# Performance work log

Measured on AMD Instinct MI355X. Metric: run time of the kernel, lower is better.

## Reference

```python
import jax, jax.numpy as jnp
import numpy as np

DIM = 128
HALF = DIM // 2
K = 8
B_TAIL = 1.0
MIN_W = 1e-3
MIN_H = 1e-3
MIN_D = 1e-3


def _fcnn(x, w1, b1, w2, b2, w3, b3):
    h = jax.nn.silu(x @ w1 + b1)
    h = jax.nn.silu(h @ w2 + b2)
    return h @ w3 + b3


def _rqs_forward(x, uw, uh, ud):
    # x: (B, D); uw/uh: (B, D, K); ud: (B, D, K-1)
    inside = (x >= -B_TAIL) & (x <= B_TAIL)
    const = np.log(np.exp(1.0 - MIN_D) - 1.0).astype(np.float32)
    ud = jnp.pad(ud, ((0, 0), (0, 0), (1, 1)), constant_values=const)

    widths = jax.nn.softmax(uw, axis=-1)
    widths = MIN_W + (1.0 - MIN_W * K) * widths
    cumw = jnp.pad(jnp.cumsum(widths, axis=-1), ((0, 0), (0, 0), (1, 0)))
    cumw = 2.0 * B_TAIL * cumw - B_TAIL
    cumw = cumw.at[..., 0].set(-B_TAIL).at[..., -1].set(B_TAIL)
    widths = cumw[..., 1:] - cumw[..., :-1]

    derivs = MIN_D + jax.nn.softplus(ud)

    heights = jax.nn.softmax(uh, axis=-1)
    heights = MIN_H + (1.0 - MIN_H * K) * heights
    cumh = jnp.pad(jnp.cumsum(heights, axis=-1), ((0, 0), (0, 0), (1, 0)))
    cumh = 2.0 * B_TAIL * cumh - B_TAIL
    cumh = cumh.at[..., 0].set(-B_TAIL).at[..., -1].set(B_TAIL)
    heights = cumh[..., 1:] - cumh[..., :-1]

    # searchsorted on cumwidths (forward direction)
    locs = cumw.at[..., -1].add(1e-6)
    idx = jnp.sum(x[..., None] >= locs, axis=-1) - 1
    idx = jnp.clip(idx, 0, K - 1)[..., None]  # (B, D, 1)

    g = lambda a: jnp.take_along_axis(a, idx, axis=-1)[..., 0]
    in_cumw = g(cumw)
    in_w = g(widths)
    in_cumh = g(cumh)
    in_h = g(heights)
    in_delta = g(heights / widths)
    d0 = g(derivs)
    d1 = g(derivs[..., 1:])

    theta = (x - in_cumw) / in_w
    t1mt = theta * (1.0 - theta)
    numer = in_h * (in_delta * theta * theta + d0 * t1mt)
    denom = in_delta + (d0 + d1 - 2.0 * in_delta) * t1mt
    out = in_cumh + numer / denom
    dnum = in_delta * in_delta * (d1 * theta * theta + 2.0 * in_delta * t1mt + d0 * (1.0 - theta) ** 2)
    lad = jnp.log(dnum) - 2.0 * jnp.log(denom)

    out = jnp.where(inside, out, x)
    lad = jnp.where(inside, lad, 0.0)
    return out, lad


def _forward(x, f1, f2):
    lower, upper = x[:, :HALF], x[:, HALF:]
    out = _fcnn(lower, *f1).reshape(-1, DIM - HALF, 3 * K - 1)
    W, H, D = out[..., :K], out[..., K:2 * K], out[..., 2 * K:]
    upper, ld1 = _rqs_forward(upper, W, H, D)
    out = _fcnn(upper, *f2).reshape(-1, HALF, 3 * K - 1)
    W, H, D = out[..., :K], out[..., K:2 * K], out[..., 2 * K:]
    lower, ld2 = _rqs_forward(lower, W, H, D)
    log_det = jnp.sum(ld1, axis=1) + jnp.sum(ld2, axis=1)
    return jnp.concatenate([lower, upper], axis=1), log_det


def setup_inputs() -> dict:
    key = jax.random.key(0)
    ks = jax.random.split(key, 13)
    batch = 32768
    x = jax.random.uniform(ks[0], (batch, DIM), jnp.float32, -1.2, 1.2)
    hd = 512
    out_dim = (3 * K - 1) * HALF  # 1472

    def lin(k, fan_in, fan_out):
        bound = 1.0 / np.sqrt(fan_in)
        kw, kb = jax.random.split(k)
        w = jax.random.uniform(kw, (fan_in, fan_out), jnp.float32, -bound, bound)
        b = jax.random.uniform(kb, (fan_out,), jnp.float32, -bound, bound)
        return w, b

    f1_w1, f1_b1 = lin(ks[1], HALF, hd)
    f1_w2, f1_b2 = lin(ks[2], hd, hd)
    f1_w3, f1_b3 = lin(ks[3], hd, out_dim)
    f2_w1, f2_b1 = lin(ks[4], HALF, hd)
    f2_w2, f2_b2 = lin(ks[5], hd, hd)
    f2_w3, f2_b3 = lin(ks[6], hd, out_dim)
    return dict(x=x,
                f1_w1=f1_w1, f1_b1=f1_b1, f1_w2=f1_w2, f1_b2=f1_b2, f1_w3=f1_w3, f1_b3=f1_b3,
                f2_w1=f2_w1, f2_b1=f2_b1, f2_w2=f2_w2, f2_b2=f2_b2, f2_w3=f2_w3, f2_b3=f2_b3)


def reference(x, f1_w1, f1_b1, f1_w2, f1_b2, f1_w3, f1_b3,
              f2_w1, f2_b1, f2_w2, f2_b2, f2_w3, f2_b3):
    f1 = (f1_w1, f1_b1, f1_w2, f1_b2, f1_w3, f1_b3)
    f2 = (f2_w1, f2_b1, f2_w2, f2_b2, f2_w3, f2_b3)
    return _forward(x, f1, f2)
```

## Files before the change

kernel.cpp:

```cpp
#include <hip/hip_runtime.h>

#define DIM 128
#define HALF 64

typedef __attribute__((ext_vector_type(8))) short bf16x8;
typedef __attribute__((ext_vector_type(4))) float f32x4;

static __device__ __forceinline__ float bf2f(unsigned int u16) {
    unsigned int v = u16 << 16;
    return __builtin_bit_cast(float, v);
}
static __device__ __forceinline__ unsigned short f2bf(float f) {
    unsigned int u = __builtin_bit_cast(unsigned int, f);
    unsigned int r = 0x7fffu + ((u >> 16) & 1u);
    u += r;
    return (unsigned short)(u >> 16);
}

static __device__ __forceinline__ void gload_lds16(const void* gptr, void* ldsptr) {
    __builtin_amdgcn_global_load_lds(
        (const __attribute__((address_space(1))) unsigned int*)(uintptr_t)gptr,
        (__attribute__((address_space(3))) unsigned int*)(unsigned int)(uintptr_t)ldsptr,
        16, 0, 0);
}

#define RAW_BARRIER()  __builtin_amdgcn_s_barrier()
#define SCHED_FENCE()  __builtin_amdgcn_sched_barrier(0)
#define WAIT_VM(n)     asm volatile("s_waitcnt vmcnt(" #n ")" ::: "memory")


__global__ void conv_lower_kernel(const float* __restrict__ x,
                                  unsigned short* __restrict__ xl, int batch) {
    int i = blockIdx.x * 256 + threadIdx.x;
    if (i < batch * HALF) {
        int r = i >> 6, c = i & 63;
        xl[i] = f2bf(x[(size_t)r * DIM + c]);
    }
}

struct TransDesc {
    const float* src[6];
    unsigned short* dst[6];
};

__global__ void transpose_all_kernel(TransDesc d) {
    __shared__ float tile[32][33];
    int z = blockIdx.z;
    int K, BN, BK, Nin, pad24;
    switch (z) {
        case 0: case 3: K = 64;  BK = 2;  BN = 16; Nin = 512;  pad24 = 0; break;
        case 1: case 4: K = 512; BK = 16; BN = 16; Nin = 512;  pad24 = 0; break;
        default:        K = 512; BK = 16; BN = 48; Nin = 1472; pad24 = 1; break;
    }
    int bn = blockIdx.x, bk = blockIdx.y;
    if (bn >= BN || bk >= BK) return;
    const float* w = d.src[z];
    unsigned short* wt = d.dst[z];
    int tx = threadIdx.x, ty = threadIdx.y;
#pragma unroll
    for (int i = 0; i < 4; ++i) {
        int k = bk * 32 + ty + 8 * i;
        int n = bn * 32 + tx;
        float v = 0.f;
        if (pad24) {
            int g = n / 24, cc = n % 24;
            if (cc < 23) v = w[(size_t)k * Nin + (g * 23 + cc)];
        } else {
            v = w[(size_t)k * Nin + n];
        }
        tile[ty + 8 * i][tx] = v;
    }
    __syncthreads();
#pragma unroll
    for (int i = 0; i < 4; ++i) {
        int n = bn * 32 + ty + 8 * i;
        int k = bk * 32 + tx;
        wt[(size_t)n * K + k] = f2bf(tile[tx][ty + 8 * i]);
    }
}

template <bool SILU, int NT>
__global__ __launch_bounds__(256, 4) void gemm_bf16_kernel(
    const unsigned short* __restrict__ A, const unsigned short* __restrict__ Bt,
    const float* __restrict__ bias, unsigned short* __restrict__ C,
    int M, int N, int K) {
    __shared__ __align__(16) unsigned char smem[34816];
    unsigned short* a_lds = (unsigned short*)smem;
    unsigned short* b_lds = (unsigned short*)(smem + 16384);
    unsigned short* cbuf = (unsigned short*)smem;

    const int t = threadIdx.x;
    const int lane = t & 63;
    const int wid = t >> 6;
    const int wr = wid >> 1, wc = wid & 1;

    const int nwg = gridDim.x;
    const int b = blockIdx.x;
    const int id = ((nwg & 7) == 0) ? ((b & 7) * (nwg >> 3) + (b >> 3)) : b;
    const int m0 = (id / NT) * 128;
    const int n0 = (id % NT) * 128;

    const int l15 = lane & 15;
    const int l4 = lane >> 4;
    const int srow = lane >> 3;
    const int sseg = lane & 7;
    const int sseg_swz = sseg ^ srow;
    const int rswz = (l15 & 7) * 8;

    f32x4 acc[4][4] = {};

    for (int kt = 0; kt < K; kt += 64) {
#pragma unroll
        for (int i = 0; i < 4; ++i) {
            int chunk = wid * 4 + i;
            int row = chunk * 8 + srow;
            const unsigned short* gA = A + (size_t)(m0 + row) * K + kt + sseg_swz * 8;
            const unsigned short* gB = Bt + (size_t)(n0 + row) * K + kt + sseg_swz * 8;
            gload_lds16(gA, &a_lds[chunk * 512]);
            gload_lds16(gB, &b_lds[chunk * 512]);
        }
        __syncthreads();
#pragma unroll
        for (int k0 = 0; k0 < 2; ++k0) {
            bf16x8 af[4], bfv[4];
#pragma unroll
            for (int f = 0; f < 4; ++f) {
                int col = (k0 * 32 + l4 * 8) ^ rswz;
                af[f] = *reinterpret_cast<const bf16x8*>(
                    &a_lds[(wr * 64 + f * 16 + l15) * 64 + col]);
                bfv[f] = *reinterpret_cast<const bf16x8*>(
                    &b_lds[(wc * 64 + f * 16 + l15) * 64 + col]);
            }
#pragma unroll
            for (int fm = 0; fm < 4; ++fm)
#pragma unroll
                for (int fn = 0; fn < 4; ++fn)
                    acc[fm][fn] = __builtin_amdgcn_mfma_f32_16x16x32_bf16(
                        af[fm], bfv[fn], acc[fm][fn], 0, 0, 0);
        }
        __syncthreads();
    }

    float bv[4];
#pragma unroll
    for (int fn = 0; fn < 4; ++fn) bv[fn] = bias[n0 + wc * 64 + fn * 16 + l15];
#pragma unroll
    for (int fm = 0; fm < 4; ++fm) {
#pragma unroll
        for (int r = 0; r < 4; ++r) {
            int rl = wr * 64 + fm * 16 + l4 * 4 + r;
#pragma unroll
            for (int fn = 0; fn < 4; ++fn) {
                float v = acc[fm][fn][r] + bv[fn];
                if (SILU) v = v / (1.f + __expf(-v));
                cbuf[rl * 136 + wc * 64 + fn * 16 + l15] = f2bf(v);
            }
        }
    }
    __syncthreads();
#pragma unroll
    for (int p = 0; p < 8; ++p) {
        int unit = p * 256 + t;
        int row = unit >> 4, seg = unit & 15;
        uint4 v = *reinterpret_cast<const uint4*>(&cbuf[row * 136 + seg * 8]);
        *reinterpret_cast<uint4*>(&C[(size_t)(m0 + row) * N + n0 + seg * 8]) = v;
    }
}

template <bool SILU, bool PAD24, int NT>
__global__ __launch_bounds__(512, 1) void gemm256_kernel(
    const unsigned short* __restrict__ A, const unsigned short* __restrict__ Bt,
    const float* __restrict__ bias, unsigned short* __restrict__ C,
    int M, int N, int K) {
    __shared__ __align__(16) unsigned short lds[256 * 264];

    const int t = threadIdx.x;
    const int lane = t & 63;
    const int wid = t >> 6;
    const int wr = wid >> 2;
    const int wc = wid & 3;
    const int l15 = lane & 15;
    const int l4 = lane >> 4;

    const int nwg = gridDim.x;
    const int b = blockIdx.x;
    const int id = ((nwg & 7) == 0) ? ((b & 7) * (nwg >> 3) + (b >> 3)) : b;
    const int m0 = (id / NT) * 256;
    const int n0 = (id % NT) * 256;

    const int nkt = K >> 5;

    int srow0 = t >> 2;
    int srow1 = (512 + t) >> 2;
    int sslot0 = (t & 3) ^ ((srow0 >> 1) & 3);
    int sslot1 = (t & 3) ^ ((srow1 >> 1) & 3);
    const int wbase0 = wid * 512;
    const int wbase1 = 4096 + wid * 512;

    f32x4 acc[8][4] = {};

    auto stage = [&](int u) {
        const int bi = (u & 3) * 16384;
        const unsigned short* Au = A + (size_t)m0 * K + u * 32;
        const unsigned short* Bu = Bt + (size_t)n0 * K + u * 32;
        gload_lds16(Au + (size_t)srow0 * K + sslot0 * 8, &lds[bi + wbase0]);
        gload_lds16(Au + (size_t)srow1 * K + sslot1 * 8, &lds[bi + wbase1]);
        gload_lds16(Bu + (size_t)srow0 * K + sslot0 * 8, &lds[bi + 8192 + wbase0]);
        gload_lds16(Bu + (size_t)srow1 * K + sslot1 * 8, &lds[bi + 8192 + wbase1]);
    };

    stage(0); stage(1); stage(2);
    WAIT_VM(8);
    RAW_BARRIER();
    SCHED_FENCE();

    for (int kt = 0; kt < nkt; ++kt) {
        if (kt + 3 < nkt) stage(kt + 3);

        const unsigned short* ab = &lds[(kt & 3) * 16384];
        const unsigned short* bb = ab + 8192;

        bf16x8 af[8], bfv[4];
#pragma unroll
        for (int f = 0; f < 8; ++f) {
            int row = wr * 128 + f * 16 + l15;
            int col = (l4 ^ ((row >> 1) & 3)) * 8;
            af[f] = *reinterpret_cast<const bf16x8*>(&ab[row * 32 + col]);
        }
#pragma unroll
        for (int f = 0; f < 4; ++f) {
            int row = wc * 64 + f * 16 + l15;
            int col = (l4 ^ ((row >> 1) & 3)) * 8;
            bfv[f] = *reinterpret_cast<const bf16x8*>(&bb[row * 32 + col]);
        }

        __builtin_amdgcn_s_setprio(1);
#pragma unroll
        for (int fm = 0; fm < 8; ++fm)
#pragma unroll
            for (int fn = 0; fn < 4; ++fn)
                acc[fm][fn] = __builtin_amdgcn_mfma_f32_16x16x32_bf16(
                    af[fm], bfv[fn], acc[fm][fn], 0, 0, 0);
        __builtin_amdgcn_s_setprio(0);

        if (kt < nkt - 3) { WAIT_VM(8); }
        else if (kt == nkt - 3) { WAIT_VM(4); }
        else if (kt == nkt - 2) { WAIT_VM(0); }
        RAW_BARRIER();
        SCHED_FENCE();
    }

    unsigned short* cbuf = lds;
    float bv[4];
#pragma unroll
    for (int fn = 0; fn < 4; ++fn) {
        int n = n0 + wc * 64 + fn * 16 + l15;
        if (PAD24) {
            int g = n / 24, cc = n % 24;
            bv[fn] = (cc < 23) ? bias[g * 23 + cc] : 0.f;
        } else {
            bv[fn] = bias[n];
        }
    }
#pragma unroll
    for (int fm = 0; fm < 8; ++fm) {
#pragma unroll
        for (int r = 0; r < 4; ++r) {
            int rl = wr * 128 + fm * 16 + l4 * 4 + r;
#pragma unroll
            for (int fn = 0; fn < 4; ++fn) {
                float v = acc[fm][fn][r] + bv[fn];
                if (SILU) v = v / (1.f + __expf(-v));
                cbuf[rl * 264 + wc * 64 + fn * 16 + l15] = f2bf(v);
            }
        }
    }
    __syncthreads();
#pragma unroll
    for (int p = 0; p < 16; ++p) {
        int unit = p * 512 + t;
        int row = unit >> 5, seg = unit & 31;
        uint4 v = *reinterpret_cast<const uint4*>(&cbuf[row * 264 + seg * 8]);
        *reinterpret_cast<uint4*>(&C[(size_t)(m0 + row) * N + n0 + seg * 8]) = v;
    }
}

__global__ __launch_bounds__(256, 1) void rqs_kernel(
        const float* __restrict__ x,
        const unsigned short* __restrict__ P,
        float* __restrict__ out, unsigned short* __restrict__ out_bf,
        float* __restrict__ ld_buf, float* __restrict__ logdet_out,
        int xoff, int pass, int batch) {
    const int wid = threadIdx.x >> 6;
    const int lane = threadIdx.x & 63;
    const int r = blockIdx.x * 4 + wid;
    if (r >= batch) return;

    const uint4* pv = reinterpret_cast<const uint4*>(P + (size_t)r * 1536 + lane * 24);
    uint4 q0 = pv[0], q1 = pv[1], q2 = pv[2];

    float W[8], H[8], Dv[7];
    {
        unsigned int a;
        a = q0.x; W[0] = bf2f(a & 0xffff); W[1] = bf2f(a >> 16);
        a = q0.y; W[2] = bf2f(a & 0xffff); W[3] = bf2f(a >> 16);
        a = q0.z; W[4] = bf2f(a & 0xffff); W[5] = bf2f(a >> 16);
        a = q0.w; W[6] = bf2f(a & 0xffff); W[7] = bf2f(a >> 16);
        a = q1.x; H[0] = bf2f(a & 0xffff); H[1] = bf2f(a >> 16);
        a = q1.y; H[2] = bf2f(a & 0xffff); H[3] = bf2f(a >> 16);
        a = q1.z; H[4] = bf2f(a & 0xffff); H[5] = bf2f(a >> 16);
        a = q1.w; H[6] = bf2f(a & 0xffff); H[7] = bf2f(a >> 16);
        a = q2.x; Dv[0] = bf2f(a & 0xffff); Dv[1] = bf2f(a >> 16);
        a = q2.y; Dv[2] = bf2f(a & 0xffff); Dv[3] = bf2f(a >> 16);
        a = q2.z; Dv[4] = bf2f(a & 0xffff); Dv[5] = bf2f(a >> 16);
        a = q2.w; Dv[6] = bf2f(a & 0xffff);
    }

    float cw[9], ch[9];
    {
        float m = W[0];
#pragma unroll
        for (int i = 1; i < 8; ++i) m = fmaxf(m, W[i]);
        float e[8], s = 0.f;
#pragma unroll
        for (int i = 0; i < 8; ++i) { e[i] = __expf(W[i] - m); s += e[i]; }
        float inv = __builtin_amdgcn_rcpf(s), cum = 0.f;
        cw[0] = -1.f;
#pragma unroll
        for (int i = 0; i < 8; ++i) {
            cum += 0.001f + 0.992f * e[i] * inv;
            cw[i + 1] = 2.f * cum - 1.f;
        }
        cw[8] = 1.f;
    }
    {
        float m = H[0];
#pragma unroll
        for (int i = 1; i < 8; ++i) m = fmaxf(m, H[i]);
        float e[8], s = 0.f;
#pragma unroll
        for (int i = 0; i < 8; ++i) { e[i] = __expf(H[i] - m); s += e[i]; }
        float inv = __builtin_amdgcn_rcpf(s), cum = 0.f;
        ch[0] = -1.f;
#pragma unroll
        for (int i = 0; i < 8; ++i) {
            cum += 0.001f + 0.992f * e[i] * inv;
            ch[i + 1] = 2.f * cum - 1.f;
        }
        ch[8] = 1.f;
    }
    float dv[9];
    dv[0] = 1.f; dv[8] = 1.f;
#pragma unroll
    for (int i = 0; i < 7; ++i) {
        float d = Dv[i];
        dv[i + 1] = 0.001f + fmaxf(d, 0.f) + __logf(1.f + __expf(-fabsf(d)));
    }

    const float xv = x[(size_t)r * DIM + xoff + lane];

    int cnt = (xv >= -1.f) ? 1 : 0;
#pragma unroll
    for (int i = 1; i < 8; ++i) cnt += (xv >= cw[i]) ? 1 : 0;
    cnt += (xv >= 1.000001f) ? 1 : 0;
    int idx = cnt - 1;
    idx = idx < 0 ? 0 : (idx > 7 ? 7 : idx);

    float in_cumw = -1.f, in_w = 1.f, in_cumh = -1.f, in_h = 1.f, d0 = 1.f, d1 = 1.f;
#pragma unroll
    for (int i = 0; i < 8; ++i) {
        bool s = (idx == i);
        float wi = cw[i + 1] - cw[i];
        float hi = ch[i + 1] - ch[i];
        in_cumw = s ? cw[i] : in_cumw;
        in_w = s ? wi : in_w;
        in_cumh = s ? ch[i] : in_cumh;
        in_h = s ? hi : in_h;
        d0 = s ? dv[i] : d0;
        d1 = s ? dv[i + 1] : d1;
    }

    float rw = __builtin_amdgcn_rcpf(in_w);
    float in_delta = in_h * rw;
    float theta = (xv - in_cumw) * rw;
    float omt = 1.f - theta;
    float t1mt = theta * omt;
    float numer = in_h * (in_delta * theta * theta + d0 * t1mt);
    float denom = in_delta + (d0 + d1 - 2.f * in_delta) * t1mt;
    float rd = __builtin_amdgcn_rcpf(denom);
    float outv = in_cumh + numer * rd;
    float dnum = in_delta * in_delta *
                 (d1 * theta * theta + 2.f * in_delta * t1mt + d0 * omt * omt);
    float lad = __logf(dnum * rd * rd);

    bool inside = (xv >= -1.f) && (xv <= 1.f);
    outv = inside ? outv : xv;
    lad = inside ? lad : 0.f;

    out[(size_t)r * DIM + xoff + lane] = outv;
    if (pass == 1) out_bf[(size_t)r * HALF + lane] = f2bf(outv);

#pragma unroll
    for (int off = 32; off > 0; off >>= 1) lad += __shfl_xor(lad, off);

    if (lane == 0) {
        if (pass == 1) ld_buf[r] = lad;
        else logdet_out[r] = lad + ld_buf[r];
    }
}


extern "C" void kernel_launch(void* const* d_in, const int* in_sizes, int n_in,
                              void* d_out, int out_size, void* d_ws, size_t ws_size,
                              hipStream_t stream) {
    const float* x = (const float*)d_in[0];
    const float* f1w1 = (const float*)d_in[1];
    const float* f1b1 = (const float*)d_in[2];
    const float* f1w2 = (const float*)d_in[3];
    const float* f1b2 = (const float*)d_in[4];
    const float* f1w3 = (const float*)d_in[5];
    const float* f1b3 = (const float*)d_in[6];
    const float* f2w1 = (const float*)d_in[7];
    const float* f2b1 = (const float*)d_in[8];
    const float* f2w2 = (const float*)d_in[9];
    const float* f2b2 = (const float*)d_in[10];
    const float* f2w3 = (const float*)d_in[11];
    const float* f2b3 = (const float*)d_in[12];
    const int batch = in_sizes[0] / DIM;
    float* out = (float*)d_out;

    char* ws = (char*)d_ws;
    size_t off = 0;
    auto alloc = [&](size_t bytes) -> void* {
        void* p = ws + off;
        off += (bytes + 255) & ~(size_t)255;
        return p;
    };
    unsigned short* xl = (unsigned short*)alloc((size_t)batch * 64 * 2);
    unsigned short* ub = (unsigned short*)alloc((size_t)batch * 64 * 2);
    unsigned short* w1t1 = (unsigned short*)alloc(512 * 64 * 2);
    unsigned short* w2t1 = (unsigned short*)alloc(512 * 512 * 2);
    unsigned short* w3t1 = (unsigned short*)alloc(1536 * 512 * 2);
    unsigned short* w1t2 = (unsigned short*)alloc(512 * 64 * 2);
    unsigned short* w2t2 = (unsigned short*)alloc(512 * 512 * 2);
    unsigned short* w3t2 = (unsigned short*)alloc(1536 * 512 * 2);
    unsigned short* h1 = (unsigned short*)alloc((size_t)batch * 512 * 2);
    unsigned short* h2 = (unsigned short*)alloc((size_t)batch * 512 * 2);
    unsigned short* par = (unsigned short*)alloc((size_t)batch * 1536 * 2);
    float* ld1 = (float*)alloc((size_t)batch * 4);
    (void)ws_size; (void)n_in; (void)out_size;

    conv_lower_kernel<<<(batch * 64 + 255) / 256, 256, 0, stream>>>(x, xl, batch);
    TransDesc td;
    td.src[0] = f1w1; td.dst[0] = w1t1;
    td.src[1] = f1w2; td.dst[1] = w2t1;
    td.src[2] = f1w3; td.dst[2] = w3t1;
    td.src[3] = f2w1; td.dst[3] = w1t2;
    td.src[4] = f2w2; td.dst[4] = w2t2;
    td.src[5] = f2w3; td.dst[5] = w3t2;
    transpose_all_kernel<<<dim3(48, 16, 6), dim3(32, 8), 0, stream>>>(td);

    const int MB128 = batch / 128;
    const int MB256 = batch / 256;
    gemm_bf16_kernel<true, 4><<<MB128 * 4, 256, 0, stream>>>(xl, w1t1, f1b1, h1, batch, 512, 64);
    gemm256_kernel<true, false, 2><<<MB256 * 2, 512, 0, stream>>>(h1, w2t1, f1b2, h2, batch, 512, 512);
    gemm256_kernel<false, true, 6><<<MB256 * 6, 512, 0, stream>>>(h2, w3t1, f1b3, par, batch, 1536, 512);
    rqs_kernel<<<batch / 4, 256, 0, stream>>>(x, par, out, ub, ld1, nullptr, HALF, 1, batch);
    gemm_bf16_kernel<true, 4><<<MB128 * 4, 256, 0, stream>>>(ub, w1t2, f2b1, h1, batch, 512, 64);
    gemm256_kernel<true, false, 2><<<MB256 * 2, 512, 0, stream>>>(h1, w2t2, f2b2, h2, batch, 512, 512);
    gemm256_kernel<false, true, 6><<<MB256 * 6, 512, 0, stream>>>(h2, w3t2, f2b3, par, batch, 1536, 512);
    rqs_kernel<<<batch / 4, 256, 0, stream>>>(x, par, out, nullptr, ld1, out + (size_t)batch * DIM, 0, 2, batch);
}
```

Baseline: 356.9 us.

## Restructure GEMM main loop into split-phase triple-buffered pipeline with interleaved staging

Replaces the 4-stage LDS ring (prefetch depth 3) with a 3-buffer ring (prefetch depth 2). Each k-step is split into two halves. The A and B global-to-LDS loads for step kt+2 are issued separately between the halves, with extra barriers and lgkmcnt waits so LDS fragment reads overlap MFMA work. LDS fragment offsets are now precomputed once outside the loop. The intent is finer interleaving of memory and compute and lower address arithmetic, at the cost of more barriers per iteration and a shallower prefetch.

```diff
diff --git a/kernel.cpp b/kernel.cpp
--- a/kernel.cpp
+++ b/kernel.cpp
@@ -26,6 +26,7 @@
 
 #define RAW_BARRIER()  __builtin_amdgcn_s_barrier()
 #define SCHED_FENCE()  __builtin_amdgcn_sched_barrier(0)
+#define WAIT_LGKM0()   asm volatile("s_waitcnt lgkmcnt(0)" ::: "memory")
 #define WAIT_VM(n)     asm volatile("s_waitcnt vmcnt(" #n ")" ::: "memory")
 
 
@@ -190,62 +191,88 @@
 
     const int nkt = K >> 5;
 
-    int srow0 = t >> 2;
-    int srow1 = (512 + t) >> 2;
-    int sslot0 = (t & 3) ^ ((srow0 >> 1) & 3);
-    int sslot1 = (t & 3) ^ ((srow1 >> 1) & 3);
+    const int arow0 = t >> 2;
+    const int arow1 = 128 + (t >> 2);
+    const int aslot0 = (t & 3) ^ ((arow0 >> 1) & 3);
+    const int aslot1 = (t & 3) ^ ((arow1 >> 1) & 3);
     const int wbase0 = wid * 512;
     const int wbase1 = 4096 + wid * 512;
 
+    int aoff[8], boff[4];
+#pragma unroll
+    for (int f = 0; f < 8; ++f) {
+        int row = wr * 128 + f * 16 + l15;
+        aoff[f] = row * 32 + ((l4 ^ ((row >> 1) & 3)) * 8);
+    }
+#pragma unroll
+    for (int g = 0; g < 4; ++g) {
+        int row = wc * 64 + g * 16 + l15;
+        boff[g] = 8192 + row * 32 + ((l4 ^ ((row >> 1) & 3)) * 8);
+    }
+
     f32x4 acc[8][4] = {};
 
-    auto stage = [&](int u) {
-        const int bi = (u & 3) * 16384;
+    auto stageA = [&](int u) {
+        const int bi = (u % 3) * 16384;
         const unsigned short* Au = A + (size_t)m0 * K + u * 32;
+        gload_lds16(Au + (size_t)arow0 * K + aslot0 * 8, &lds[bi + wbase0]);
+        gload_lds16(Au + (size_t)arow1 * K + aslot1 * 8, &lds[bi + wbase1]);
+    };
+    auto stageB = [&](int u) {
+        const int bi = (u % 3) * 16384 + 8192;
         const unsigned short* Bu = Bt + (size_t)n0 * K + u * 32;
-        gload_lds16(Au + (size_t)srow0 * K + sslot0 * 8, &lds[bi + wbase0]);
-        gload_lds16(Au + (size_t)srow1 * K + sslot1 * 8, &lds[bi + wbase1]);
-        gload_lds16(Bu + (size_t)srow0 * K + sslot0 * 8, &lds[bi + 8192 + wbase0]);
-        gload_lds16(Bu + (size_t)srow1 * K + sslot1 * 8, &lds[bi + 8192 + wbase1]);
+        gload_lds16(Bu + (size_t)arow0 * K + aslot0 * 8, &lds[bi + wbase0]);
+        gload_lds16(Bu + (size_t)arow1 * K + aslot1 * 8, &lds[bi + wbase1]);
     };
 
-    stage(0); stage(1); stage(2);
-    WAIT_VM(8);
+    stageA(0); stageB(0); stageA(1); stageB(1);
+    WAIT_VM(4);
     RAW_BARRIER();
     SCHED_FENCE();
 
     for (int kt = 0; kt < nkt; ++kt) {
-        if (kt + 3 < nkt) stage(kt + 3);
-
-        const unsigned short* ab = &lds[(kt & 3) * 16384];
-        const unsigned short* bb = ab + 8192;
-
-        bf16x8 af[8], bfv[4];
-#pragma unroll
-        for (int f = 0; f < 8; ++f) {
-            int row = wr * 128 + f * 16 + l15;
-            int col = (l4 ^ ((row >> 1) & 3)) * 8;
-            af[f] = *reinterpret_cast<const bf16x8*>(&ab[row * 32 + col]);
-        }
-#pragma unroll
-        for (int f = 0; f < 4; ++f) {
-            int row = wc * 64 + f * 16 + l15;
-            int col = (l4 ^ ((row >> 1) & 3)) * 8;
-            bfv[f] = *reinterpret_cast<const bf16x8*>(&bb[row * 32 + col]);
-        }
-
+        const int bi = (kt % 3) * 16384;
+        const bool st = (kt + 2 < nkt);
+
+        bf16x8 bfv[4], af[4];
+#pragma unroll
+        for (int g = 0; g < 4; ++g)
+            bfv[g] = *reinterpret_cast<const bf16x8*>(&lds[bi + boff[g]]);
+#pragma unroll
+        for (int f = 0; f < 4; ++f)
+            af[f] = *reinterpret_cast<const bf16x8*>(&lds[bi + aoff[f]]);
+        if (st) stageA(kt + 2);
+        RAW_BARRIER();
+        WAIT_LGKM0();
+        SCHED_FENCE();
         __builtin_amdgcn_s_setprio(1);
 #pragma unroll
-        for (int fm = 0; fm < 8; ++fm)
+        for (int fm = 0; fm < 4; ++fm)
 #pragma unroll
             for (int fn = 0; fn < 4; ++fn)
                 acc[fm][fn] = __builtin_amdgcn_mfma_f32_16x16x32_bf16(
                     af[fm], bfv[fn], acc[fm][fn], 0, 0, 0);
         __builtin_amdgcn_s_setprio(0);
-
-        if (kt < nkt - 3) { WAIT_VM(8); }
-        else if (kt == nkt - 3) { WAIT_VM(4); }
-        else if (kt == nkt - 2) { WAIT_VM(0); }
+        RAW_BARRIER();
+        SCHED_FENCE();
+
+        bf16x8 af2[4];
+#pragma unroll
+        for (int f = 0; f < 4; ++f)
+            af2[f] = *reinterpret_cast<const bf16x8*>(&lds[bi + aoff[4 + f]]);
+        if (st) stageB(kt + 2);
+        RAW_BARRIER();
+        WAIT_LGKM0();
+        SCHED_FENCE();
+        __builtin_amdgcn_s_setprio(1);
+#pragma unroll
+        for (int fm = 0; fm < 4; ++fm)
+#pragma unroll
+            for (int fn = 0; fn < 4; ++fn)
+                acc[4 + fm][fn] = __builtin_amdgcn_mfma_f32_16x16x32_bf16(
+                    af2[fm], bfv[fn], acc[4 + fm][fn], 0, 0, 0);
+        __builtin_amdgcn_s_setprio(0);
+        if (st) { WAIT_VM(4); } else { WAIT_VM(0); }
         RAW_BARRIER();
         SCHED_FENCE();
     }
```

After: 378.4 us. 1.06x slower.
